# Kernel optimization log

Hardware: AMD Instinct MI355X
Metric: run time of the kernel (lower is better)

## Reference

```python
import jax, jax.numpy as jnp
import numpy as np

N_NODES = 100000
N_EDGES = 600000
D = 128


def setup_inputs() -> dict:
    key = jax.random.key(0)
    k1, k2, k3, k4, k5 = jax.random.split(key, 5)
    feature = jax.random.normal(k1, (N_NODES, D), dtype=jnp.float32)
    edge_index = jax.random.randint(k2, (2, N_EDGES), 0, N_NODES, dtype=jnp.int64)
    scale = 1.0 / np.sqrt(D)
    # PyG SAGEConv params: lin_l (applied to aggregated neighbors, with bias),
    # lin_r (applied to root/self features, no bias).
    W_l = jax.random.uniform(k3, (D, D), dtype=jnp.float32, minval=-scale, maxval=scale)
    b_l = jax.random.uniform(k4, (D,), dtype=jnp.float32, minval=-scale, maxval=scale)
    W_r = jax.random.uniform(k5, (D, D), dtype=jnp.float32, minval=-scale, maxval=scale)
    return {"feature": feature, "edge_index": edge_index, "W_l": W_l, "b_l": b_l, "W_r": W_r}


def reference(feature, edge_index, W_l, b_l, W_r):
    # SAGEConv with mean aggregation:
    #   out_i = lin_l( mean_{j in N(i)} x_j ) + lin_r( x_i )
    src, dst = edge_index[0], edge_index[1]
    msgs = feature[src]  # [E, D] gather of source-node features
    agg = jax.ops.segment_sum(msgs, dst, num_segments=feature.shape[0])  # [N, D]
    deg = jax.ops.segment_sum(jnp.ones((edge_index.shape[1],), dtype=feature.dtype),
                              dst, num_segments=feature.shape[0])  # [N]
    agg = agg / jnp.maximum(deg, 1.0)[:, None]  # mean; isolated nodes -> 0
    return agg @ W_l.T + b_l + feature @ W_r.T
```

## Files before the change

### kernel.cpp

```cpp
#include <hip/hip_runtime.h>

#define N_NODES 100000
#define N_EDGES 600000
#define DIM 128
#define PAD 64

__global__ __launch_bounds__(256) void detect_kernel(
    const unsigned* __restrict__ w, unsigned* __restrict__ flag) {
  unsigned v = 0;
  for (int i = threadIdx.x; i < 2048; i += 256) v |= w[2 * i + 1];
  unsigned long long b = __ballot(v != 0);
  if ((threadIdx.x & 63) == 0 && b) atomicOr(flag, 1u);
}

__global__ __launch_bounds__(256) void sage_fill(
    const int* __restrict__ ei32,
    const long long* __restrict__ ei64,
    const unsigned* __restrict__ flag,
    int* __restrict__ cursor,
    int* __restrict__ adj) {
  int e = blockIdx.x * blockDim.x + threadIdx.x;
  if (e >= N_EDGES) return;
  const bool i32 = (*flag != 0u);
  int s, d;
  if (i32) { s = ei32[e];       d = ei32[N_EDGES + e]; }
  else     { s = (int)ei64[e];  d = (int)ei64[N_EDGES + e]; }
  int slot = atomicAdd(&cursor[d], 1);
  if (slot < PAD) adj[(size_t)d * PAD + slot] = s;
}

__global__ __launch_bounds__(256) void sage_pull(
    const float* __restrict__ feat,
    const int* __restrict__ adj,
    const int* __restrict__ cursor,
    float* __restrict__ agg) {
  int node = blockIdx.x * 8 + (threadIdx.x >> 5);
  if (node >= N_NODES) return;
  int hl = threadIdx.x & 31;
  int deg = cursor[node];
  int cnt = min(deg, PAD);
  const int* __restrict__ row = adj + (size_t)node * PAD;
  int sv = row[hl];
  float ax = 0.f, ay = 0.f, az = 0.f, aw = 0.f;
  int iter = min(cnt, 32);
  int d = 0;
  for (; d + 1 < iter; d += 2) {
    int s0 = __shfl(sv, d, 32);
    int s1 = __shfl(sv, d + 1, 32);
    float4 v0 = ((const float4*)(feat + (size_t)s0 * DIM))[hl];
    float4 v1 = ((const float4*)(feat + (size_t)s1 * DIM))[hl];
    ax += v0.x; ay += v0.y; az += v0.z; aw += v0.w;
    ax += v1.x; ay += v1.y; az += v1.z; aw += v1.w;
  }
  if (d < iter) {
    int s = __shfl(sv, d, 32);
    float4 v = ((const float4*)(feat + (size_t)s * DIM))[hl];
    ax += v.x; ay += v.y; az += v.z; aw += v.w;
  }
  if (cnt > 32) {
    for (int k = 32; k < cnt; ++k) {
      int s = row[k];
      float4 v = ((const float4*)(feat + (size_t)s * DIM))[hl];
      ax += v.x; ay += v.y; az += v.z; aw += v.w;
    }
  }
  float inv = 1.0f / fmaxf((float)deg, 1.0f);
  ((float4*)(agg + (size_t)node * DIM))[hl] =
      make_float4(ax * inv, ay * inv, az * inv, aw * inv);
}

#define BM 128
#define BN 128
#define BK 32
#define XLD (BM + 4)
#define WLD (BN + 4)

__global__ __launch_bounds__(256, 2) void sage_gemm(
    const float* __restrict__ feat,
    const float* __restrict__ agg,
    const float* __restrict__ Wl,
    const float* __restrict__ bl,
    const float* __restrict__ Wr,
    float* __restrict__ out) {

  __shared__ float Xs[BK][XLD];
  __shared__ float Ws[BK][WLD];

  const int tid = threadIdx.x;
  const int brow = blockIdx.x * BM;

  const int r0 = (tid & 15) * 4;
  const int c0 = (tid >> 4) * 4;

  float acc[8][8];
#pragma unroll
  for (int i = 0; i < 8; i++)
#pragma unroll
    for (int j = 0; j < 8; j++) acc[i][j] = 0.f;

  for (int kb = 0; kb < 2 * DIM; kb += BK) {
    const bool isAgg = (kb < DIM);
    const int kglob = isAgg ? kb : kb - DIM;
    const float* __restrict__ Xsrc = isAgg ? agg : feat;
    const float* __restrict__ Wsrc = isAgg ? Wl : Wr;

#pragma unroll
    for (int j = 0; j < 4; j++) {
      int f4 = j * 256 + tid;
      int r = f4 >> 3;
      int k4 = (f4 & 7) * 4;
      int row = brow + r;
      float4 v = make_float4(0.f, 0.f, 0.f, 0.f);
      if (row < N_NODES) v = *(const float4*)&Xsrc[(size_t)row * DIM + kglob + k4];
      Xs[k4 + 0][r] = v.x; Xs[k4 + 1][r] = v.y;
      Xs[k4 + 2][r] = v.z; Xs[k4 + 3][r] = v.w;
    }
#pragma unroll
    for (int j = 0; j < 4; j++) {
      int f4 = j * 256 + tid;
      int d = f4 >> 3;
      int k4 = (f4 & 7) * 4;
      float4 v = *(const float4*)&Wsrc[(size_t)d * DIM + kglob + k4];
      Ws[k4 + 0][d] = v.x; Ws[k4 + 1][d] = v.y;
      Ws[k4 + 2][d] = v.z; Ws[k4 + 3][d] = v.w;
    }
    __syncthreads();

#pragma unroll 8
    for (int kk = 0; kk < BK; kk++) {
      float4 a0 = *(const float4*)&Xs[kk][r0];
      float4 a1 = *(const float4*)&Xs[kk][r0 + 64];
      float4 b0 = *(const float4*)&Ws[kk][c0];
      float4 b1 = *(const float4*)&Ws[kk][c0 + 64];
      float a[8] = {a0.x, a0.y, a0.z, a0.w, a1.x, a1.y, a1.z, a1.w};
      float b[8] = {b0.x, b0.y, b0.z, b0.w, b1.x, b1.y, b1.z, b1.w};
#pragma unroll
      for (int i = 0; i < 8; i++)
#pragma unroll
        for (int j = 0; j < 8; j++) acc[i][j] = fmaf(a[i], b[j], acc[i][j]);
    }
    __syncthreads();
  }

  float4 bias0 = *(const float4*)&bl[c0];
  float4 bias1 = *(const float4*)&bl[c0 + 64];
  float bb[8] = {bias0.x, bias0.y, bias0.z, bias0.w,
                 bias1.x, bias1.y, bias1.z, bias1.w};

#pragma unroll
  for (int i = 0; i < 8; i++) {
    int row = brow + ((i < 4) ? (r0 + i) : (64 + r0 + i - 4));
    if (row < N_NODES) {
      float* op = out + (size_t)row * DIM;
      float4 o0, o1;
      o0.x = acc[i][0] + bb[0]; o0.y = acc[i][1] + bb[1];
      o0.z = acc[i][2] + bb[2]; o0.w = acc[i][3] + bb[3];
      o1.x = acc[i][4] + bb[4]; o1.y = acc[i][5] + bb[5];
      o1.z = acc[i][6] + bb[6]; o1.w = acc[i][7] + bb[7];
      *(float4*)(op + c0) = o0;
      *(float4*)(op + c0 + 64) = o1;
    }
  }
}

__global__ __launch_bounds__(256) void sage_scatter(
    const float* __restrict__ feat,
    const int* __restrict__ ei32,
    const long long* __restrict__ ei64,
    const unsigned* __restrict__ flag,
    float* __restrict__ agg,
    float* __restrict__ deg,
    int nWaves) {
  int wave = (blockIdx.x * blockDim.x + threadIdx.x) >> 6;
  int lane = threadIdx.x & 63;
  const bool i32 = (*flag != 0u);
  for (int e = wave; e < N_EDGES; e += nWaves) {
    int s, d;
    if (i32) { s = ei32[e];      d = ei32[N_EDGES + e]; }
    else     { s = (int)ei64[e]; d = (int)ei64[N_EDGES + e]; }
    float2 v = ((const float2*)(feat + (size_t)s * DIM))[lane];
    float* a = agg + (size_t)d * DIM + lane * 2;
    unsafeAtomicAdd(a, v.x);
    unsafeAtomicAdd(a + 1, v.y);
    if (lane == 0) unsafeAtomicAdd(deg + d, 1.0f);
  }
}

__global__ __launch_bounds__(256) void sage_norm(
    float* __restrict__ agg, const float* __restrict__ deg) {
  int i = blockIdx.x * blockDim.x + threadIdx.x;
  if (i >= N_NODES * DIM) return;
  int n = i >> 7;
  agg[i] *= 1.0f / fmaxf(deg[n], 1.0f);
}

extern "C" void kernel_launch(void* const* d_in, const int* in_sizes, int n_in,
                              void* d_out, int out_size, void* d_ws, size_t ws_size,
                              hipStream_t stream) {
  const float* feat = (const float*)d_in[0];
  const int* ei32 = (const int*)d_in[1];
  const long long* ei64 = (const long long*)d_in[1];
  const unsigned* eiw = (const unsigned*)d_in[1];
  const float* Wl = (const float*)d_in[2];
  const float* bl = (const float*)d_in[3];
  const float* Wr = (const float*)d_in[4];
  float* out = (float*)d_out;

  const size_t needPull = (16 + (size_t)N_NODES + (size_t)N_NODES * PAD) * 4
                        + (size_t)N_NODES * DIM * 4;

  const int gblocks = (N_NODES + BM - 1) / BM;

  if (ws_size >= needPull) {
    unsigned* flag = (unsigned*)d_ws;
    int* cursor = (int*)d_ws + 16;
    int* adj = cursor + N_NODES;
    float* agg = (float*)(adj + (size_t)N_NODES * PAD);
    hipMemsetAsync(d_ws, 0, (16 + (size_t)N_NODES) * 4, stream);
    detect_kernel<<<1, 256, 0, stream>>>(eiw, flag);
    sage_fill<<<(N_EDGES + 255) / 256, 256, 0, stream>>>(ei32, ei64, flag, cursor, adj);
    sage_pull<<<(N_NODES + 7) / 8, 256, 0, stream>>>(feat, adj, cursor, agg);
    sage_gemm<<<gblocks, 256, 0, stream>>>(feat, agg, Wl, bl, Wr, out);
  } else {
    unsigned* flag = (unsigned*)d_ws;
    float* agg = (float*)d_ws + 16;
    float* deg = agg + (size_t)N_NODES * DIM;
    hipMemsetAsync(d_ws, 0, (16 + (size_t)N_NODES * DIM + N_NODES) * 4, stream);
    detect_kernel<<<1, 256, 0, stream>>>(eiw, flag);
    const int sblocks = 2048;
    sage_scatter<<<sblocks, 256, 0, stream>>>(feat, ei32, ei64, flag, agg, deg, sblocks * 4);
    sage_norm<<<(N_NODES * DIM + 255) / 256, 256, 0, stream>>>(agg, deg);
    sage_gemm<<<gblocks, 256, 0, stream>>>(feat, agg, Wl, bl, Wr, out);
  }
}
```

Measured before the change: 280.3 us.

## Replace FP32 SIMT GEMM with split-bf16 MFMA GEMM using swizzled LDS

Rewrites the dense linear-layer GEMM to use bf16 MFMA instructions. Each fp32 operand is split into a high bf16 part plus a bf16 residual, and three MFMAs per tile are issued to keep close to fp32 accuracy. Operands are staged in XOR-swizzled LDS with a K tile of 64, and each wave computes a 64x64 output block. The goal is to move the FMA-bound GEMM onto matrix cores. The cost is extra conversion work, the three-pass multiply, less coalesced scalar output stores, and no overlap between loads and compute.

```diff
diff --git a/kernel.cpp b/kernel.cpp
--- a/kernel.cpp
+++ b/kernel.cpp
@@ -4,6 +4,9 @@
 #define N_EDGES 600000
 #define DIM 128
 #define PAD 64
+
+typedef __attribute__((ext_vector_type(8))) short short8;
+typedef __attribute__((ext_vector_type(4))) float f32x4;
 
 __global__ __launch_bounds__(256) void detect_kernel(
     const unsigned* __restrict__ w, unsigned* __restrict__ flag) {
@@ -69,13 +72,15 @@
       make_float4(ax * inv, ay * inv, az * inv, aw * inv);
 }
 
-#define BM 128
-#define BN 128
-#define BK 32
-#define XLD (BM + 4)
-#define WLD (BN + 4)
-
-__global__ __launch_bounds__(256, 2) void sage_gemm(
+#define GBM 128
+#define GBK 64
+
+__device__ __forceinline__ unsigned bf16_rne_hi(float x) {
+  unsigned u = __float_as_uint(x);
+  return (u + 0x7FFFu + ((u >> 16) & 1u)) & 0xFFFF0000u;
+}
+
+__global__ __launch_bounds__(256, 2) void sage_gemm_mfma(
     const float* __restrict__ feat,
     const float* __restrict__ agg,
     const float* __restrict__ Wl,
@@ -83,82 +88,123 @@
     const float* __restrict__ Wr,
     float* __restrict__ out) {
 
-  __shared__ float Xs[BK][XLD];
-  __shared__ float Ws[BK][WLD];
+  __shared__ ushort XhL[GBM * GBK];
+  __shared__ ushort XlL[GBM * GBK];
+  __shared__ ushort WhL[DIM * GBK];
+  __shared__ ushort WloL[DIM * GBK];
 
   const int tid = threadIdx.x;
-  const int brow = blockIdx.x * BM;
-
-  const int r0 = (tid & 15) * 4;
-  const int c0 = (tid >> 4) * 4;
-
-  float acc[8][8];
-#pragma unroll
-  for (int i = 0; i < 8; i++)
-#pragma unroll
-    for (int j = 0; j < 8; j++) acc[i][j] = 0.f;
-
-  for (int kb = 0; kb < 2 * DIM; kb += BK) {
-    const bool isAgg = (kb < DIM);
-    const int kglob = isAgg ? kb : kb - DIM;
-    const float* __restrict__ Xsrc = isAgg ? agg : feat;
-    const float* __restrict__ Wsrc = isAgg ? Wl : Wr;
-
-#pragma unroll
-    for (int j = 0; j < 4; j++) {
-      int f4 = j * 256 + tid;
-      int r = f4 >> 3;
-      int k4 = (f4 & 7) * 4;
-      int row = brow + r;
+  const int brow = blockIdx.x * GBM;
+  const int w = tid >> 6;
+  const int lane = tid & 63;
+  const int l15 = lane & 15;
+  const int lgrp = lane >> 4;
+  const int wr = (w >> 1) * 64;
+  const int wc = (w & 1) * 64;
+
+  f32x4 acc[4][4];
+#pragma unroll
+  for (int i = 0; i < 4; i++)
+#pragma unroll
+    for (int j = 0; j < 4; j++) acc[i][j] = (f32x4){0.f, 0.f, 0.f, 0.f};
+
+  for (int kb = 0; kb < 4; kb++) {
+    const float* __restrict__ Xsrc = (kb < 2) ? agg : feat;
+    const float* __restrict__ Wsrc = (kb < 2) ? Wl : Wr;
+    const int koff = (kb & 1) * GBK;
+
+    __syncthreads();
+#pragma unroll
+    for (int i = 0; i < 8; i++) {
+      int f4 = i * 256 + tid;
+      int r = f4 >> 4;
+      int k4 = (f4 & 15) * 4;
+      int grow = brow + r;
       float4 v = make_float4(0.f, 0.f, 0.f, 0.f);
-      if (row < N_NODES) v = *(const float4*)&Xsrc[(size_t)row * DIM + kglob + k4];
-      Xs[k4 + 0][r] = v.x; Xs[k4 + 1][r] = v.y;
-      Xs[k4 + 2][r] = v.z; Xs[k4 + 3][r] = v.w;
-    }
-#pragma unroll
-    for (int j = 0; j < 4; j++) {
-      int f4 = j * 256 + tid;
-      int d = f4 >> 3;
-      int k4 = (f4 & 7) * 4;
-      float4 v = *(const float4*)&Wsrc[(size_t)d * DIM + kglob + k4];
-      Ws[k4 + 0][d] = v.x; Ws[k4 + 1][d] = v.y;
-      Ws[k4 + 2][d] = v.z; Ws[k4 + 3][d] = v.w;
+      if (grow < N_NODES) v = *(const float4*)&Xsrc[(size_t)grow * DIM + koff + k4];
+      unsigned h0 = bf16_rne_hi(v.x), h1 = bf16_rne_hi(v.y);
+      unsigned h2 = bf16_rne_hi(v.z), h3 = bf16_rne_hi(v.w);
+      float lx = v.x - __uint_as_float(h0);
+      float ly = v.y - __uint_as_float(h1);
+      float lz = v.z - __uint_as_float(h2);
+      float lw = v.w - __uint_as_float(h3);
+      uint2 hp, lp;
+      hp.x = (h0 >> 16) | h1;
+      hp.y = (h2 >> 16) | h3;
+      lp.x = (__float_as_uint(lx) >> 16) | (__float_as_uint(ly) & 0xFFFF0000u);
+      lp.y = (__float_as_uint(lz) >> 16) | (__float_as_uint(lw) & 0xFFFF0000u);
+      int idx = r * GBK + (k4 ^ ((r & 7) << 3));
+      *(uint2*)&XhL[idx] = hp;
+      *(uint2*)&XlL[idx] = lp;
+    }
+#pragma unroll
+    for (int i = 0; i < 8; i++) {
+      int f4 = i * 256 + tid;
+      int c = f4 >> 4;
+      int k4 = (f4 & 15) * 4;
+      float4 v = *(const float4*)&Wsrc[(size_t)c * DIM + koff + k4];
+      unsigned h0 = bf16_rne_hi(v.x), h1 = bf16_rne_hi(v.y);
+      unsigned h2 = bf16_rne_hi(v.z), h3 = bf16_rne_hi(v.w);
+      float lx = v.x - __uint_as_float(h0);
+      float ly = v.y - __uint_as_float(h1);
+      float lz = v.z - __uint_as_float(h2);
+      float lw = v.w - __uint_as_float(h3);
+      uint2 hp, lp;
+      hp.x = (h0 >> 16) | h1;
+      hp.y = (h2 >> 16) | h3;
+      lp.x = (__float_as_uint(lx) >> 16) | (__float_as_uint(ly) & 0xFFFF0000u);
+      lp.y = (__float_as_uint(lz) >> 16) | (__float_as_uint(lw) & 0xFFFF0000u);
+      int idx = c * GBK + (k4 ^ ((c & 7) << 3));
+      *(uint2*)&WhL[idx] = hp;
+      *(uint2*)&WloL[idx] = lp;
     }
     __syncthreads();
 
-#pragma unroll 8
-    for (int kk = 0; kk < BK; kk++) {
-      float4 a0 = *(const float4*)&Xs[kk][r0];
-      float4 a1 = *(const float4*)&Xs[kk][r0 + 64];
-      float4 b0 = *(const float4*)&Ws[kk][c0];
-      float4 b1 = *(const float4*)&Ws[kk][c0 + 64];
-      float a[8] = {a0.x, a0.y, a0.z, a0.w, a1.x, a1.y, a1.z, a1.w};
-      float b[8] = {b0.x, b0.y, b0.z, b0.w, b1.x, b1.y, b1.z, b1.w};
-#pragma unroll
-      for (int i = 0; i < 8; i++)
-#pragma unroll
-        for (int j = 0; j < 8; j++) acc[i][j] = fmaf(a[i], b[j], acc[i][j]);
-    }
-    __syncthreads();
-  }
-
-  float4 bias0 = *(const float4*)&bl[c0];
-  float4 bias1 = *(const float4*)&bl[c0 + 64];
-  float bb[8] = {bias0.x, bias0.y, bias0.z, bias0.w,
-                 bias1.x, bias1.y, bias1.z, bias1.w};
-
-#pragma unroll
-  for (int i = 0; i < 8; i++) {
-    int row = brow + ((i < 4) ? (r0 + i) : (64 + r0 + i - 4));
-    if (row < N_NODES) {
-      float* op = out + (size_t)row * DIM;
-      float4 o0, o1;
-      o0.x = acc[i][0] + bb[0]; o0.y = acc[i][1] + bb[1];
-      o0.z = acc[i][2] + bb[2]; o0.w = acc[i][3] + bb[3];
-      o1.x = acc[i][4] + bb[4]; o1.y = acc[i][5] + bb[5];
-      o1.z = acc[i][6] + bb[6]; o1.w = acc[i][7] + bb[7];
-      *(float4*)(op + c0) = o0;
-      *(float4*)(op + c0 + 64) = o1;
+#pragma unroll
+    for (int ks = 0; ks < 2; ks++) {
+      const int k0 = ks * 32 + lgrp * 8;
+      short8 ah[4], al[4], bh[4], blo[4];
+#pragma unroll
+      for (int f = 0; f < 4; f++) {
+        int ar = wr + f * 16 + l15;
+        int aidx = ar * GBK + (k0 ^ ((ar & 7) << 3));
+        ah[f] = *(const short8*)&XhL[aidx];
+        al[f] = *(const short8*)&XlL[aidx];
+        int bc = wc + f * 16 + l15;
+        int bidx = bc * GBK + (k0 ^ ((bc & 7) << 3));
+        bh[f] = *(const short8*)&WhL[bidx];
+        blo[f] = *(const short8*)&WloL[bidx];
+      }
+#pragma unroll
+      for (int fi = 0; fi < 4; fi++)
+#pragma unroll
+        for (int fj = 0; fj < 4; fj++) {
+          acc[fi][fj] = __builtin_amdgcn_mfma_f32_16x16x32_bf16(
+              ah[fi], bh[fj], acc[fi][fj], 0, 0, 0);
+          acc[fi][fj] = __builtin_amdgcn_mfma_f32_16x16x32_bf16(
+              ah[fi], blo[fj], acc[fi][fj], 0, 0, 0);
+          acc[fi][fj] = __builtin_amdgcn_mfma_f32_16x16x32_bf16(
+              al[fi], bh[fj], acc[fi][fj], 0, 0, 0);
+        }
+    }
+  }
+
+  float bias[4];
+#pragma unroll
+  for (int fj = 0; fj < 4; fj++) bias[fj] = bl[wc + fj * 16 + l15];
+
+#pragma unroll
+  for (int fi = 0; fi < 4; fi++) {
+    int rb = brow + wr + fi * 16 + lgrp * 4;
+#pragma unroll
+    for (int r = 0; r < 4; r++) {
+      int row = rb + r;
+      if (row < N_NODES) {
+        float* op = out + (size_t)row * DIM + wc;
+#pragma unroll
+        for (int fj = 0; fj < 4; fj++)
+          op[fj * 16 + l15] = acc[fi][fj][r] + bias[fj];
+      }
     }
   }
 }
@@ -209,7 +255,7 @@
   const size_t needPull = (16 + (size_t)N_NODES + (size_t)N_NODES * PAD) * 4
                         + (size_t)N_NODES * DIM * 4;
 
-  const int gblocks = (N_NODES + BM - 1) / BM;
+  const int gblocks = (N_NODES + GBM - 1) / GBM;
 
   if (ws_size >= needPull) {
     unsigned* flag = (unsigned*)d_ws;
@@ -220,7 +266,7 @@
     detect_kernel<<<1, 256, 0, stream>>>(eiw, flag);
     sage_fill<<<(N_EDGES + 255) / 256, 256, 0, stream>>>(ei32, ei64, flag, cursor, adj);
     sage_pull<<<(N_NODES + 7) / 8, 256, 0, stream>>>(feat, adj, cursor, agg);
-    sage_gemm<<<gblocks, 256, 0, stream>>>(feat, agg, Wl, bl, Wr, out);
+    sage_gemm_mfma<<<gblocks, 256, 0, stream>>>(feat, agg, Wl, bl, Wr, out);
   } else {
     unsigned* flag = (unsigned*)d_ws;
     float* agg = (float*)d_ws + 16;
@@ -230,6 +276,6 @@
     const int sblocks = 2048;
     sage_scatter<<<sblocks, 256, 0, stream>>>(feat, ei32, ei64, flag, agg, deg, sblocks * 4);
     sage_norm<<<(N_NODES * DIM + 255) / 256, 256, 0, stream>>>(agg, deg);
-    sage_gemm<<<gblocks, 256, 0, stream>>>(feat, agg, Wl, bl, Wr, out);
-  }
-}
+    sage_gemm_mfma<<<gblocks, 256, 0, stream>>>(feat, agg, Wl, bl, Wr, out);
+  }
+}
```

After: 230.7 us. -17.7%, faster.
